# Kernel tuning notes

Hardware: AMD Instinct MI355X
Metric: run time of the kernel (lower is better)

## Reference

```python
import jax, jax.numpy as jnp
import numpy as np

B, T, D, H, F = 256, 128, 64, 512, 256


def setup_inputs() -> dict:
    key = jax.random.key(0)
    ks = jax.random.split(key, 4)
    return {
        "observations": jax.random.normal(ks[0], (B, T, D), dtype=jnp.float32),
        "Wx": jax.random.normal(ks[1], (D, 4 * H), dtype=jnp.float32) / np.sqrt(D),
        "Wh": jax.random.normal(ks[2], (H, 4 * H), dtype=jnp.float32) / np.sqrt(H),
        "b": jnp.zeros((4 * H,), dtype=jnp.float32),
        "Wd": jax.random.normal(ks[3], (H, F), dtype=jnp.float32) / np.sqrt(H),
        "bd": jnp.zeros((F,), dtype=jnp.float32),
    }


def reference(observations, Wx, Wh, b, Wd, bd):
    # observations: [B, T, D]. Flax nnx.LSTMCell gate order: i, f, g, o;
    # input kernels have no bias, hidden kernels carry the bias.
    batch = observations.shape[0]
    hidden = Wh.shape[0]
    # Precompute input projections for all timesteps in one big GEMM: [T, B, 4H]
    x_proj = jnp.einsum("btd,dg->tbg", observations, Wx)

    def step(carry, xp_t):
        c, h = carry
        gates = xp_t + h @ Wh + b  # [B, 4H]
        i, f, g, o = jnp.split(gates, 4, axis=-1)
        i = jax.nn.sigmoid(i)
        f = jax.nn.sigmoid(f)
        g = jnp.tanh(g)
        o = jax.nn.sigmoid(o)
        c_new = f * c + i * g
        h_new = o * jnp.tanh(c_new)
        return (c_new, h_new), None

    c0 = jnp.zeros((batch, hidden), dtype=observations.dtype)
    h0 = jnp.zeros((batch, hidden), dtype=observations.dtype)
    (c_last, h_last), _ = jax.lax.scan(step, (c0, h0), x_proj)
    return jax.nn.relu(h_last @ Wd + bd)
```

## Files before the change

kernel.cpp:

```cpp
#include <hip/hip_runtime.h>


#define WH_S 524
#define WX_S 72
#define HT_S 524

typedef __attribute__((ext_vector_type(4))) _Float16 f16x4;
typedef __attribute__((ext_vector_type(4))) float    f32x4;
typedef __attribute__((ext_vector_type(2))) unsigned long long u64x2;
typedef unsigned long long u64;

__device__ __forceinline__ float sigm(float x)  { return 1.f / (1.f + __expf(-x)); }
__device__ __forceinline__ float tanh_(float x) { float e = __expf(2.f * x); return 1.f - 2.f / (e + 1.f); }

__device__ __forceinline__ u64x2 ld128_cc(const void* p) {
    u64x2 v;
    asm volatile("global_load_dwordx4 %0, %1, off sc0 sc1" : "=v"(v) : "v"(p));
    return v;
}
__device__ __forceinline__ unsigned ldflag_cc(const unsigned* p) {
    unsigned v;
    asm volatile("global_load_dword %0, %1, off sc0 sc1\n\ts_waitcnt vmcnt(0)"
                 : "=v"(v) : "v"(p) : "memory");
    return v;
}
__device__ __forceinline__ void stflag_cc(unsigned* p, unsigned v) {
    asm volatile("global_store_dword %0, %1, off sc0 sc1" :: "v"(p), "v"(v) : "memory");
}

#define MFMA16(w, a, c) __builtin_amdgcn_mfma_f32_16x16x16f16((w), (a), (c), 0, 0, 0)

__launch_bounds__(256, 1)
__global__ void lstm_persist(const float* __restrict__ obs,
                             const float* __restrict__ Wx,
                             const float* __restrict__ Wh,
                             const float* __restrict__ bvec,
                             u64* __restrict__ hbuf,
                             unsigned* __restrict__ flg)
{
    __shared__ _Float16 sbuf[128 * WH_S];

    const int tid = threadIdx.x, lane = tid & 63, wid = tid >> 6;
    const int grp = blockIdx.x & 15, slc = blockIdx.x >> 4;
    const int l15 = lane & 15, l16 = lane >> 4;
    const int c0 = (wid << 5) + l15, c1 = c0 + 16;

    for (int idx = tid; idx < 512 * 128; idx += 256) {
        int k = idx >> 7, c = idx & 127;
        int u = ((c >> 5) << 3) | (c & 7);
        int g = (((c >> 4) & 1) << 1) | ((c >> 3) & 1);
        sbuf[c * WH_S + k] = (_Float16)Wh[k * 2048 + (g << 9) + (slc << 5) + u];
    }
    __syncthreads();
    f16x4 wf0[32], wf1[32];
    #pragma unroll
    for (int kk = 0; kk < 32; ++kk) {
        wf0[kk] = *(const f16x4*)&sbuf[c0 * WH_S + (kk << 4) + (l16 << 2)];
        wf1[kk] = *(const f16x4*)&sbuf[c1 * WH_S + (kk << 4) + (l16 << 2)];
    }
    __syncthreads();
    for (int idx = tid; idx < 64 * 128; idx += 256) {
        int k = idx >> 7, c = idx & 127;
        int u = ((c >> 5) << 3) | (c & 7);
        int g = (((c >> 4) & 1) << 1) | ((c >> 3) & 1);
        sbuf[c * WX_S + k] = (_Float16)Wx[k * 2048 + (g << 9) + (slc << 5) + u];
    }
    __syncthreads();
    f16x4 xw0[4], xw1[4];
    #pragma unroll
    for (int kx = 0; kx < 4; ++kx) {
        xw0[kx] = *(const f16x4*)&sbuf[c0 * WX_S + (kx << 4) + (l16 << 2)];
        xw1[kx] = *(const f16x4*)&sbuf[c1 * WX_S + (kx << 4) + (l16 << 2)];
    }
    __syncthreads();
    _Float16* const sh = sbuf;

    const int brow = (grp << 4) + l15;
    const int ub   = (wid << 3) + ((l16 & 1) << 2);
    f32x4 bia[4];
    #pragma unroll
    for (int g = 0; g < 4; ++g)
        bia[g] = *(const f32x4*)(bvec + (g << 9) + (slc << 5) + ub);

    const int r_ld  = (wid << 2) + l16;
    const int ch16  = l15;
    const int hstore_idx = (brow << 7) + (slc << 3) + (wid << 1) + (l16 & 1);
    unsigned* const gflg = flg + (grp << 4);

    float c_reg[4] = {0.f, 0.f, 0.f, 0.f};

    for (int t = 0; t < 128; ++t) {
        const u64* hc = hbuf + ((t & 1) ? 32768 : 0);
        u64*       hn = hbuf + ((t & 1) ? 0 : 32768);

        f16x4 xf[4];
        const float* op = obs + ((brow << 7) + t) * 64;
        #pragma unroll
        for (int kx = 0; kx < 4; ++kx) {
            f32x4 ov = *(const f32x4*)(op + (kx << 4) + (l16 << 2));
            #pragma unroll
            for (int e = 0; e < 4; ++e) xf[kx][e] = (_Float16)ov[e];
        }
        __builtin_amdgcn_sched_barrier(0);

        if (t) {
            if (wid == 0) {
                const unsigned tgt = (unsigned)t;
                for (;;) {
                    unsigned f = ldflag_cc(gflg + l15);
                    if (__all((int)(f >= tgt))) break;
                    __builtin_amdgcn_s_sleep(1);
                }
            }
            __syncthreads();
        }

        const u64* hrow = hc + (((grp << 4) + r_ld) << 7) + (ch16 << 1);
        u64x2 hv4[4];
        #pragma unroll
        for (int j = 0; j < 4; ++j) hv4[j] = ld128_cc(hrow + (j << 5));
        asm volatile("s_waitcnt vmcnt(0)" ::: "memory");
        #pragma unroll
        for (int j = 0; j < 4; ++j) {
            *(u64*)&sh[r_ld * HT_S + (j << 7) + (ch16 << 3)]     = hv4[j][0];
            *(u64*)&sh[r_ld * HT_S + (j << 7) + (ch16 << 3) + 4] = hv4[j][1];
        }
        __syncthreads();

        f32x4 a00 = {0.f,0.f,0.f,0.f}, a01 = {0.f,0.f,0.f,0.f};
        f32x4 a10 = {0.f,0.f,0.f,0.f}, a11 = {0.f,0.f,0.f,0.f};

        #pragma unroll
        for (int kx = 0; kx < 4; ++kx) {
            if (kx & 1) { a01 = MFMA16(xw0[kx], xf[kx], a01); a11 = MFMA16(xw1[kx], xf[kx], a11); }
            else        { a00 = MFMA16(xw0[kx], xf[kx], a00); a10 = MFMA16(xw1[kx], xf[kx], a10); }
        }
        #pragma unroll
        for (int kk = 0; kk < 32; ++kk) {
            f16x4 af = *(const f16x4*)&sh[l15 * HT_S + (kk << 4) + (l16 << 2)];
            if (kk & 1) { a01 = MFMA16(wf0[kk], af, a01); a11 = MFMA16(wf1[kk], af, a11); }
            else        { a00 = MFMA16(wf0[kk], af, a00); a10 = MFMA16(wf1[kk], af, a10); }
        }
        f32x4 t0 = a00 + a01, t1 = a10 + a11;

        f32x4 r0, r1;
        #pragma unroll
        for (int rr = 0; rr < 4; ++rr) {
            r0[rr] = __shfl_xor(t0[rr], 32, 64);
            r1[rr] = __shfl_xor(t1[rr], 32, 64);
        }
        const bool low = (l16 < 2);
        f16x4 hv;
        #pragma unroll
        for (int rr = 0; rr < 4; ++rr) {
            float I  = low ? t0[rr] : r0[rr];
            float Fv = low ? r0[rr] : t0[rr];
            float G  = low ? t1[rr] : r1[rr];
            float O  = low ? r1[rr] : t1[rr];
            I  = sigm (I  + bia[0][rr]);
            Fv = sigm (Fv + bia[1][rr]);
            G  = tanh_(G  + bia[2][rr]);
            O  = sigm (O  + bia[3][rr]);
            float cn  = Fv * c_reg[rr] + I * G;
            c_reg[rr] = cn;
            hv[rr] = (_Float16)(O * tanh_(cn));
        }
        if (low)
            __hip_atomic_store(hn + hstore_idx, __builtin_bit_cast(u64, hv),
                               __ATOMIC_RELAXED, __HIP_MEMORY_SCOPE_AGENT);

        if (t < 127) {
            asm volatile("s_waitcnt vmcnt(0)" ::: "memory");
            __syncthreads();
            if (tid == 0)
                stflag_cc(gflg + slc, (unsigned)(t + 1));
        }
    }
}

__launch_bounds__(256)
__global__ void final_proj(const _Float16* __restrict__ hlast,
                           const float* __restrict__ Wd,
                           const float* __restrict__ bd,
                           float* __restrict__ out)
{
    __shared__ float shm[2048];
    const int tid = threadIdx.x;
    const int rb  = blockIdx.x;
    for (int idx = tid; idx < 2048; idx += 256)
        shm[idx] = (float)hlast[(rb << 2) * 512 + idx];
    __syncthreads();
    float a0 = 0.f, a1 = 0.f, a2 = 0.f, a3 = 0.f;
    for (int k = 0; k < 512; ++k) {
        float w = Wd[(k << 8) + tid];
        a0 += shm[k] * w; a1 += shm[512 + k] * w; a2 += shm[1024 + k] * w; a3 += shm[1536 + k] * w;
    }
    float bb = bd[tid];
    float v0 = a0 + bb, v1 = a1 + bb, v2 = a2 + bb, v3 = a3 + bb;
    out[((rb << 2) + 0) * 256 + tid] = v0 > 0.f ? v0 : 0.f;
    out[((rb << 2) + 1) * 256 + tid] = v1 > 0.f ? v1 : 0.f;
    out[((rb << 2) + 2) * 256 + tid] = v2 > 0.f ? v2 : 0.f;
    out[((rb << 2) + 3) * 256 + tid] = v3 > 0.f ? v3 : 0.f;
}

extern "C" void kernel_launch(void* const* d_in, const int* in_sizes, int n_in,
                              void* d_out, int out_size, void* d_ws, size_t ws_size,
                              hipStream_t stream)
{
    (void)in_sizes; (void)n_in; (void)out_size; (void)ws_size;
    const float* obs = (const float*)d_in[0];
    const float* Wx  = (const float*)d_in[1];
    const float* Wh  = (const float*)d_in[2];
    const float* bv  = (const float*)d_in[3];
    const float* Wd  = (const float*)d_in[4];
    const float* bd  = (const float*)d_in[5];
    float* out = (float*)d_out;

    u64* hbuf     = (u64*)d_ws;
    unsigned* flg = (unsigned*)((char*)d_ws + 524288);

    hipMemsetAsync(d_ws, 0, 524288 + 1024, stream);

    void* args[6];
    args[0] = (void*)&obs; args[1] = (void*)&Wx; args[2] = (void*)&Wh;
    args[3] = (void*)&bv;  args[4] = (void*)&hbuf; args[5] = (void*)&flg;
    hipError_t e = hipLaunchCooperativeKernel((const void*)lstm_persist,
                                              dim3(256), dim3(256), args, 0, stream);
    if (e != hipSuccess) {
        lstm_persist<<<dim3(256), dim3(256), 0, stream>>>(obs, Wx, Wh, bv, hbuf, flg);
    }
    final_proj<<<dim3(64), dim3(256), 0, stream>>>((const _Float16*)d_ws, Wd, bd, out);
}
```

Baseline: 547.5 us.

## Use 128 blocks of 512 threads, each covering 64 hidden units

Changes the persistent LSTM decomposition from 256 blocks of 4 waves to 128 blocks of 8 waves. Each block now owns a 64-unit hidden slice, so each batch group waits on 8 flags instead of 16. The goal is to shrink the cross-block flag synchronization and halve the number of h-state readers per step. The Wh weight load is staged through shared memory in two halves, and launch bounds change to 512 threads, which raises register pressure on the 64 f16x4 weight registers each thread holds.

```diff
diff --git a/kernel.cpp b/kernel.cpp
--- a/kernel.cpp
+++ b/kernel.cpp
@@ -30,7 +30,7 @@
 
 #define MFMA16(w, a, c) __builtin_amdgcn_mfma_f32_16x16x16f16((w), (a), (c), 0, 0, 0)
 
-__launch_bounds__(256, 1)
+__launch_bounds__(512, 2)
 __global__ void lstm_persist(const float* __restrict__ obs,
                              const float* __restrict__ Wx,
                              const float* __restrict__ Wh,
@@ -43,34 +43,54 @@
     const int tid = threadIdx.x, lane = tid & 63, wid = tid >> 6;
     const int grp = blockIdx.x & 15, slc = blockIdx.x >> 4;
     const int l15 = lane & 15, l16 = lane >> 4;
-    const int c0 = (wid << 5) + l15, c1 = c0 + 16;
-
-    for (int idx = tid; idx < 512 * 128; idx += 256) {
+    const int cl0 = ((wid & 3) << 5) + l15, cl1 = cl0 + 16;
+
+    f16x4 wf0[32], wf1[32];
+    for (int idx = tid; idx < 512 * 128; idx += 512) {
         int k = idx >> 7, c = idx & 127;
         int u = ((c >> 5) << 3) | (c & 7);
         int g = (((c >> 4) & 1) << 1) | ((c >> 3) & 1);
-        sbuf[c * WH_S + k] = (_Float16)Wh[k * 2048 + (g << 9) + (slc << 5) + u];
-    }
-    __syncthreads();
-    f16x4 wf0[32], wf1[32];
-    #pragma unroll
-    for (int kk = 0; kk < 32; ++kk) {
-        wf0[kk] = *(const f16x4*)&sbuf[c0 * WH_S + (kk << 4) + (l16 << 2)];
-        wf1[kk] = *(const f16x4*)&sbuf[c1 * WH_S + (kk << 4) + (l16 << 2)];
-    }
-    __syncthreads();
-    for (int idx = tid; idx < 64 * 128; idx += 256) {
-        int k = idx >> 7, c = idx & 127;
-        int u = ((c >> 5) << 3) | (c & 7);
-        int g = (((c >> 4) & 1) << 1) | ((c >> 3) & 1);
-        sbuf[c * WX_S + k] = (_Float16)Wx[k * 2048 + (g << 9) + (slc << 5) + u];
+        sbuf[c * WH_S + k] = (_Float16)Wh[k * 2048 + (g << 9) + (slc << 6) + u];
+    }
+    __syncthreads();
+    if (wid < 4) {
+        #pragma unroll
+        for (int kk = 0; kk < 32; ++kk) {
+            wf0[kk] = *(const f16x4*)&sbuf[cl0 * WH_S + (kk << 4) + (l16 << 2)];
+            wf1[kk] = *(const f16x4*)&sbuf[cl1 * WH_S + (kk << 4) + (l16 << 2)];
+        }
+    }
+    __syncthreads();
+    for (int idx = tid; idx < 512 * 128; idx += 512) {
+        int k = idx >> 7, c = idx & 127, C = c + 128;
+        int u = ((C >> 5) << 3) | (C & 7);
+        int g = (((C >> 4) & 1) << 1) | ((C >> 3) & 1);
+        sbuf[c * WH_S + k] = (_Float16)Wh[k * 2048 + (g << 9) + (slc << 6) + u];
+    }
+    __syncthreads();
+    if (wid >= 4) {
+        #pragma unroll
+        for (int kk = 0; kk < 32; ++kk) {
+            wf0[kk] = *(const f16x4*)&sbuf[cl0 * WH_S + (kk << 4) + (l16 << 2)];
+            wf1[kk] = *(const f16x4*)&sbuf[cl1 * WH_S + (kk << 4) + (l16 << 2)];
+        }
+    }
+    __syncthreads();
+    for (int idx = tid; idx < 64 * 256; idx += 512) {
+        int k = idx >> 8, C = idx & 255;
+        int u = ((C >> 5) << 3) | (C & 7);
+        int g = (((C >> 4) & 1) << 1) | ((C >> 3) & 1);
+        sbuf[C * WX_S + k] = (_Float16)Wx[k * 2048 + (g << 9) + (slc << 6) + u];
     }
     __syncthreads();
     f16x4 xw0[4], xw1[4];
-    #pragma unroll
-    for (int kx = 0; kx < 4; ++kx) {
-        xw0[kx] = *(const f16x4*)&sbuf[c0 * WX_S + (kx << 4) + (l16 << 2)];
-        xw1[kx] = *(const f16x4*)&sbuf[c1 * WX_S + (kx << 4) + (l16 << 2)];
+    {
+        const int cg0 = (wid << 5) + l15, cg1 = cg0 + 16;
+        #pragma unroll
+        for (int kx = 0; kx < 4; ++kx) {
+            xw0[kx] = *(const f16x4*)&sbuf[cg0 * WX_S + (kx << 4) + (l16 << 2)];
+            xw1[kx] = *(const f16x4*)&sbuf[cg1 * WX_S + (kx << 4) + (l16 << 2)];
+        }
     }
     __syncthreads();
     _Float16* const sh = sbuf;
@@ -80,11 +100,11 @@
     f32x4 bia[4];
     #pragma unroll
     for (int g = 0; g < 4; ++g)
-        bia[g] = *(const f32x4*)(bvec + (g << 9) + (slc << 5) + ub);
-
-    const int r_ld  = (wid << 2) + l16;
-    const int ch16  = l15;
-    const int hstore_idx = (brow << 7) + (slc << 3) + (wid << 1) + (l16 & 1);
+        bia[g] = *(const f32x4*)(bvec + (g << 9) + (slc << 6) + ub);
+
+    const int r_ld = (wid << 1) + (lane >> 5);
+    const int ch   = lane & 31;
+    const int hstore_idx = (brow << 7) + (slc << 4) + (wid << 1) + (l16 & 1);
     unsigned* const gflg = flg + (grp << 4);
 
     float c_reg[4] = {0.f, 0.f, 0.f, 0.f};
@@ -107,7 +127,7 @@
             if (wid == 0) {
                 const unsigned tgt = (unsigned)t;
                 for (;;) {
-                    unsigned f = ldflag_cc(gflg + l15);
+                    unsigned f = ldflag_cc(gflg + (lane & 7));
                     if (__all((int)(f >= tgt))) break;
                     __builtin_amdgcn_s_sleep(1);
                 }
@@ -115,16 +135,14 @@
             __syncthreads();
         }
 
-        const u64* hrow = hc + (((grp << 4) + r_ld) << 7) + (ch16 << 1);
-        u64x2 hv4[4];
-        #pragma unroll
-        for (int j = 0; j < 4; ++j) hv4[j] = ld128_cc(hrow + (j << 5));
+        const u64* hrow = hc + (((grp << 4) + r_ld) << 7) + (ch << 1);
+        u64x2 h0 = ld128_cc(hrow);
+        u64x2 h1 = ld128_cc(hrow + 64);
         asm volatile("s_waitcnt vmcnt(0)" ::: "memory");
-        #pragma unroll
-        for (int j = 0; j < 4; ++j) {
-            *(u64*)&sh[r_ld * HT_S + (j << 7) + (ch16 << 3)]     = hv4[j][0];
-            *(u64*)&sh[r_ld * HT_S + (j << 7) + (ch16 << 3) + 4] = hv4[j][1];
-        }
+        *(u64*)&sh[r_ld * HT_S + (ch << 3)]            = h0[0];
+        *(u64*)&sh[r_ld * HT_S + (ch << 3) + 4]        = h0[1];
+        *(u64*)&sh[r_ld * HT_S + ((ch + 32) << 3)]     = h1[0];
+        *(u64*)&sh[r_ld * HT_S + ((ch + 32) << 3) + 4] = h1[1];
         __syncthreads();
 
         f32x4 a00 = {0.f,0.f,0.f,0.f}, a01 = {0.f,0.f,0.f,0.f};
@@ -225,9 +243,9 @@
     args[0] = (void*)&obs; args[1] = (void*)&Wx; args[2] = (void*)&Wh;
     args[3] = (void*)&bv;  args[4] = (void*)&hbuf; args[5] = (void*)&flg;
     hipError_t e = hipLaunchCooperativeKernel((const void*)lstm_persist,
-                                              dim3(256), dim3(256), args, 0, stream);
+                                              dim3(128), dim3(512), args, 0, stream);
     if (e != hipSuccess) {
-        lstm_persist<<<dim3(256), dim3(256), 0, stream>>>(obs, Wx, Wh, bv, hbuf, flg);
+        lstm_persist<<<dim3(128), dim3(512), 0, stream>>>(obs, Wx, Wh, bv, hbuf, flg);
     }
     final_proj<<<dim3(64), dim3(256), 0, stream>>>((const _Float16*)d_ws, Wd, bd, out);
 }
```

Measured after the change: 631.0 us. +15.2%, slower.
